# Kernel optimization log

Measured on AMD Instinct MI355X. Metric: run time of the kernel, lower is better.

## Reference

```python
import jax, jax.numpy as jnp
import numpy as np

# init_kwargs baked in as module constants
N, K, CONV_DIM = 20, 10, 512
T, ALPHA = 0.1, 0.1
BNORM = 1.0  # self.B == 2 only when N==K==5
BATCH = 256


def setup_inputs() -> dict:
    key = jax.random.key(0)
    op = jax.random.normal(key, (BATCH, N, K, 1, CONV_DIM), dtype=jnp.float32)
    return {"op": op}


def reference(op):
    # op: [B, N, K, 1, D]
    p = jnp.squeeze(op, axis=-2)                                  # [B,N,K,D]
    p = p / jnp.linalg.norm(p, axis=-1, keepdims=True)            # L2 normalize
    b = p.shape[0]
    all_p = p.reshape(b, N * K, CONV_DIM)                         # [B,NK,D] (n-major, k-minor, same as split+concat)

    # vectorized over all N*K anchors: pairwise similarities to all prototypes
    sims = jnp.einsum('bnkd,bmd->bnkm', p, all_p) / T             # [B,N,K,NK]
    self_sim = jnp.sum(p * p, axis=-1) / T                        # [B,N,K] (== 1/T after normalization)

    # denominator: sum of exp over all prototypes minus the anchor itself
    exp_term = jnp.sum(jnp.exp(sims), axis=-1) - jnp.exp(self_sim)  # [B,N,K]
    log_term = jnp.log(exp_term)

    # positive term: mean similarity to same-class prototypes excluding anchor
    pos = jnp.einsum('bnkd,bnjd->bnk', p, p) / T                  # sum over class members incl. self
    sum_term = (pos - self_sim) / (K - 1)                         # [B,N,K]

    cl_loss = jnp.sum(log_term - sum_term)                        # sums over batch and all anchors
    return ALPHA * cl_loss / (BNORM * N * K * CONV_DIM)
```

## Files before the change

kernel.cpp:

```cpp
#include <hip/hip_runtime.h>
#include <hip/hip_bf16.h>
#include <math.h>

#define BATCH   256
#define KMEM    10
#define NPROT   200
#define DDIM    512
#define TINVF   10.0f
#define KSLAB   64
#define NSLAB   (DDIM / KSLAB)
#define RPAD    256
#define ROWB    128
#define NSEG    800

typedef __attribute__((ext_vector_type(8))) short short8;
typedef __attribute__((ext_vector_type(4))) float f32x4;

__device__ __forceinline__ unsigned short f2bf(float v) {
    unsigned u = __float_as_uint(v);
    return (unsigned short)((u + 0x7fffu + ((u >> 16) & 1u)) >> 16);
}

__device__ __forceinline__ void pack16(const float4 c[4], uint4& p0, uint4& p1, float& sq) {
    union { unsigned short us[16]; uint4 u[2]; } w;
    const float* f = (const float*)c;
    #pragma unroll
    for (int e = 0; e < 16; e++) {
        float v = f[e];
        sq = fmaf(v, v, sq);
        w.us[e] = f2bf(v);
    }
    p0 = w.u[0];
    p1 = w.u[1];
}

__global__ __launch_bounds__(512, 2) void kmain(const float* __restrict__ P,
                                                float* __restrict__ partial) {
    __shared__ char  slab[2][RPAD * ROWB];
    __shared__ float normpart[NSEG];
    __shared__ float invn_s[RPAD];
    __shared__ float s1buf[2][RPAD];
    __shared__ float s2buf[2][RPAD];
    __shared__ float red[512];

    const int tid  = threadIdx.x;
    const int lane = tid & 63;
    const int wave = tid >> 6;
    const int wr   = wave >> 1;
    const int wc   = wave & 1;
    const int b    = blockIdx.x;
    const float* Pb = P + (size_t)b * NPROT * DDIM;

    for (int z = tid; z < 2 * 56 * 8; z += 512) {
        int bsel = z / (56 * 8);
        int slot = z % (56 * 8);
        int row  = NPROT + (slot >> 3);
        *(uint4*)(&slab[bsel][row * ROWB + (slot & 7) * 16]) = make_uint4(0, 0, 0, 0);
    }

    const int  idx0 = tid;
    const int  row0 = idx0 >> 2, seg0 = idx0 & 3;
    const int  idx1 = tid + 512;
    const bool has1 = (idx1 < NSEG);
    const int  row1 = idx1 >> 2, seg1 = idx1 & 3;

    float sq0 = 0.f, sq1 = 0.f;

    float4 curA[4], curB[4];
    {
        const float4* sA = (const float4*)(Pb + (size_t)row0 * DDIM + seg0 * 16);
        curA[0] = sA[0]; curA[1] = sA[1]; curA[2] = sA[2]; curA[3] = sA[3];
        if (has1) {
            const float4* sB = (const float4*)(Pb + (size_t)row1 * DDIM + seg1 * 16);
            curB[0] = sB[0]; curB[1] = sB[1]; curB[2] = sB[2]; curB[3] = sB[3];
        }
    }

    f32x4 acc[4][8];
    #pragma unroll
    for (int i = 0; i < 4; i++)
        #pragma unroll
        for (int j = 0; j < 8; j++)
            acc[i][j] = (f32x4)(0.f);

    const int swz0 = (row0 & 7) << 4;
    const int swz1 = (row1 & 7) << 4;

    for (int s = 0; s < NSLAB; s++) {
        char* buf = slab[s & 1];

        {
            uint4 p0, p1;
            pack16(curA, p0, p1, sq0);
            int byte0 = row0 * ROWB + seg0 * 32;
            *(uint4*)(&buf[(byte0     ) ^ swz0]) = p0;
            *(uint4*)(&buf[(byte0 + 16) ^ swz0]) = p1;
        }
        if (has1) {
            uint4 p0, p1;
            pack16(curB, p0, p1, sq1);
            int byte0 = row1 * ROWB + seg1 * 32;
            *(uint4*)(&buf[(byte0     ) ^ swz1]) = p0;
            *(uint4*)(&buf[(byte0 + 16) ^ swz1]) = p1;
        }
        __syncthreads();

        float4 nxtA[4], nxtB[4];
        if (s + 1 < NSLAB) {
            const float4* sA = (const float4*)(Pb + (size_t)row0 * DDIM + (s + 1) * KSLAB + seg0 * 16);
            nxtA[0] = sA[0]; nxtA[1] = sA[1]; nxtA[2] = sA[2]; nxtA[3] = sA[3];
            if (has1) {
                const float4* sB = (const float4*)(Pb + (size_t)row1 * DDIM + (s + 1) * KSLAB + seg1 * 16);
                nxtB[0] = sB[0]; nxtB[1] = sB[1]; nxtB[2] = sB[2]; nxtB[3] = sB[3];
            }
        }

        #pragma unroll
        for (int ks = 0; ks < 2; ks++) {
            const int kb = (ks * 32 + (lane >> 4) * 8) * 2;
            short8 af[4];
            #pragma unroll
            for (int i = 0; i < 4; i++) {
                int row = (wr * 4 + i) * 16 + (lane & 15);
                af[i] = *(const short8*)(&buf[(row * ROWB + kb) ^ ((row & 7) << 4)]);
            }
            #pragma unroll
            for (int j = 0; j < 8; j++) {
                int row = (wc * 8 + j) * 16 + (lane & 15);
                short8 bf = *(const short8*)(&buf[(row * ROWB + kb) ^ ((row & 7) << 4)]);
                #pragma unroll
                for (int i = 0; i < 4; i++)
                    acc[i][j] = __builtin_amdgcn_mfma_f32_16x16x32_bf16(af[i], bf, acc[i][j], 0, 0, 0);
            }
        }

        #pragma unroll
        for (int q = 0; q < 4; q++) { curA[q] = nxtA[q]; curB[q] = nxtB[q]; }
    }

    normpart[idx0] = sq0;
    if (has1) normpart[idx1] = sq1;
    __syncthreads();
    if (tid < RPAD) {
        float iv = 0.f;
        if (tid < NPROT) {
            float ns = normpart[4 * tid] + normpart[4 * tid + 1]
                     + normpart[4 * tid + 2] + normpart[4 * tid + 3];
            iv = rsqrtf(ns);
        }
        invn_s[tid] = iv;
    }
    __syncthreads();

    float ijn[8]; int jg[8], jdiv[8];
    #pragma unroll
    for (int j = 0; j < 8; j++) {
        jg[j]   = wc * 128 + j * 16 + (lane & 15);
        ijn[j]  = invn_s[jg[j]];
        jdiv[j] = jg[j] / KMEM;
    }
    #pragma unroll
    for (int i = 0; i < 4; i++) {
        #pragma unroll
        for (int r = 0; r < 4; r++) {
            const int m = wr * 64 + i * 16 + (lane >> 4) * 4 + r;
            const float im = invn_s[m];
            const int mdiv = m / KMEM;
            float s1 = 0.f, s2 = 0.f;
            #pragma unroll
            for (int j = 0; j < 8; j++) {
                float g = acc[i][j][r] * im * ijn[j];
                bool valid = (jg[j] < NPROT) && (m < NPROT) && (jg[j] != m);
                s1 += valid ? __expf(g * TINVF) : 0.f;
                s2 += (valid && (jdiv[j] == mdiv)) ? g : 0.f;
            }
            #pragma unroll
            for (int d = 1; d < 16; d <<= 1) {
                s1 += __shfl_xor(s1, d);
                s2 += __shfl_xor(s2, d);
            }
            if ((lane & 15) == 0) {
                s1buf[wc][m] = s1;
                s2buf[wc][m] = s2;
            }
        }
    }
    __syncthreads();

    float v = 0.f;
    if (tid < NPROT) {
        float S1 = s1buf[0][tid] + s1buf[1][tid];
        float S2 = s2buf[0][tid] + s2buf[1][tid];
        v = logf(S1) - S2 * (TINVF / 9.0f);
    }
    red[tid] = v;
    __syncthreads();
    for (int sx = 256; sx > 0; sx >>= 1) {
        if (tid < sx) red[tid] += red[tid + sx];
        __syncthreads();
    }
    if (tid == 0) partial[b] = red[0];
}

__global__ __launch_bounds__(256) void kfinal(const float* __restrict__ partial,
                                              float* __restrict__ out) {
    __shared__ double red[256];
    int tid = threadIdx.x;
    red[tid] = (double)partial[tid];
    __syncthreads();
    for (int sx = 128; sx > 0; sx >>= 1) {
        if (tid < sx) red[tid] += red[tid + sx];
        __syncthreads();
    }
    if (tid == 0) out[0] = (float)(red[0] * (0.1 / 102400.0));
}

extern "C" void kernel_launch(void* const* d_in, const int* in_sizes, int n_in,
                              void* d_out, int out_size, void* d_ws, size_t ws_size,
                              hipStream_t stream) {
    const float* P = (const float*)d_in[0];
    float* partial = (float*)d_ws;
    float* out     = (float*)d_out;

    kmain<<<BATCH, 512, 0, stream>>>(P, partial);
    kfinal<<<1, 256, 0, stream>>>(partial, out);
}
```

Baseline: 33.72 us.

## Split each batch element's similarity matrix across two blocks by row halves

Launches two blocks per batch element, each computing the MFMA tiles and loss terms for half of the anchor rows against all prototypes, and combines the doubled partial sums in the final reduction. This halves per-block compute and accumulator registers, and raises the occupancy hint, to increase parallelism across CUs. The cost is that both blocks load and convert the full input slab, duplicating global reads and bf16 packing work.

```diff
diff --git a/kernel.cpp b/kernel.cpp
--- a/kernel.cpp
+++ b/kernel.cpp
@@ -12,6 +12,7 @@
 #define RPAD    256
 #define ROWB    128
 #define NSEG    800
+#define NBLK    (BATCH * 2)
 
 typedef __attribute__((ext_vector_type(8))) short short8;
 typedef __attribute__((ext_vector_type(4))) float f32x4;
@@ -34,21 +35,22 @@
     p1 = w.u[1];
 }
 
-__global__ __launch_bounds__(512, 2) void kmain(const float* __restrict__ P,
+__global__ __launch_bounds__(512, 4) void kmain(const float* __restrict__ P,
                                                 float* __restrict__ partial) {
     __shared__ char  slab[2][RPAD * ROWB];
     __shared__ float normpart[NSEG];
     __shared__ float invn_s[RPAD];
-    __shared__ float s1buf[2][RPAD];
-    __shared__ float s2buf[2][RPAD];
+    __shared__ float s1buf[4][128];
+    __shared__ float s2buf[4][128];
     __shared__ float red[512];
 
     const int tid  = threadIdx.x;
     const int lane = tid & 63;
     const int wave = tid >> 6;
-    const int wr   = wave >> 1;
-    const int wc   = wave & 1;
-    const int b    = blockIdx.x;
+    const int wrh  = wave >> 2;
+    const int wcq  = wave & 3;
+    const int b    = blockIdx.x >> 1;
+    const int h    = blockIdx.x & 1;
     const float* Pb = P + (size_t)b * NPROT * DDIM;
 
     for (int z = tid; z < 2 * 56 * 8; z += 512) {
@@ -76,11 +78,11 @@
         }
     }
 
-    f32x4 acc[4][8];
+    f32x4 acc[4][4];
     #pragma unroll
     for (int i = 0; i < 4; i++)
         #pragma unroll
-        for (int j = 0; j < 8; j++)
+        for (int j = 0; j < 4; j++)
             acc[i][j] = (f32x4)(0.f);
 
     const int swz0 = (row0 & 7) << 4;
@@ -118,20 +120,22 @@
         #pragma unroll
         for (int ks = 0; ks < 2; ks++) {
             const int kb = (ks * 32 + (lane >> 4) * 8) * 2;
-            short8 af[4];
+            short8 af[4], bfr[4];
             #pragma unroll
             for (int i = 0; i < 4; i++) {
-                int row = (wr * 4 + i) * 16 + (lane & 15);
+                int row = (h * 8 + wrh * 4 + i) * 16 + (lane & 15);
                 af[i] = *(const short8*)(&buf[(row * ROWB + kb) ^ ((row & 7) << 4)]);
             }
             #pragma unroll
-            for (int j = 0; j < 8; j++) {
-                int row = (wc * 8 + j) * 16 + (lane & 15);
-                short8 bf = *(const short8*)(&buf[(row * ROWB + kb) ^ ((row & 7) << 4)]);
+            for (int j = 0; j < 4; j++) {
+                int row = (wcq * 4 + j) * 16 + (lane & 15);
+                bfr[j] = *(const short8*)(&buf[(row * ROWB + kb) ^ ((row & 7) << 4)]);
+            }
+            #pragma unroll
+            for (int j = 0; j < 4; j++)
                 #pragma unroll
                 for (int i = 0; i < 4; i++)
-                    acc[i][j] = __builtin_amdgcn_mfma_f32_16x16x32_bf16(af[i], bf, acc[i][j], 0, 0, 0);
-            }
+                    acc[i][j] = __builtin_amdgcn_mfma_f32_16x16x32_bf16(af[i], bfr[j], acc[i][j], 0, 0, 0);
         }
 
         #pragma unroll
@@ -152,10 +156,10 @@
     }
     __syncthreads();
 
-    float ijn[8]; int jg[8], jdiv[8];
-    #pragma unroll
-    for (int j = 0; j < 8; j++) {
-        jg[j]   = wc * 128 + j * 16 + (lane & 15);
+    float ijn[4]; int jg[4], jdiv[4];
+    #pragma unroll
+    for (int j = 0; j < 4; j++) {
+        jg[j]   = wcq * 64 + j * 16 + (lane & 15);
         ijn[j]  = invn_s[jg[j]];
         jdiv[j] = jg[j] / KMEM;
     }
@@ -163,12 +167,12 @@
     for (int i = 0; i < 4; i++) {
         #pragma unroll
         for (int r = 0; r < 4; r++) {
-            const int m = wr * 64 + i * 16 + (lane >> 4) * 4 + r;
+            const int m = h * 128 + wrh * 64 + i * 16 + (lane >> 4) * 4 + r;
             const float im = invn_s[m];
             const int mdiv = m / KMEM;
             float s1 = 0.f, s2 = 0.f;
             #pragma unroll
-            for (int j = 0; j < 8; j++) {
+            for (int j = 0; j < 4; j++) {
                 float g = acc[i][j][r] * im * ijn[j];
                 bool valid = (jg[j] < NPROT) && (m < NPROT) && (jg[j] != m);
                 s1 += valid ? __expf(g * TINVF) : 0.f;
@@ -180,18 +184,21 @@
                 s2 += __shfl_xor(s2, d);
             }
             if ((lane & 15) == 0) {
-                s1buf[wc][m] = s1;
-                s2buf[wc][m] = s2;
+                s1buf[wcq][m - h * 128] = s1;
+                s2buf[wcq][m - h * 128] = s2;
             }
         }
     }
     __syncthreads();
 
     float v = 0.f;
-    if (tid < NPROT) {
-        float S1 = s1buf[0][tid] + s1buf[1][tid];
-        float S2 = s2buf[0][tid] + s2buf[1][tid];
-        v = logf(S1) - S2 * (TINVF / 9.0f);
+    if (tid < 128) {
+        const int m = h * 128 + tid;
+        if (m < NPROT) {
+            float S1 = s1buf[0][tid] + s1buf[1][tid] + s1buf[2][tid] + s1buf[3][tid];
+            float S2 = s2buf[0][tid] + s2buf[1][tid] + s2buf[2][tid] + s2buf[3][tid];
+            v = logf(S1) - S2 * (TINVF / 9.0f);
+        }
     }
     red[tid] = v;
     __syncthreads();
@@ -199,14 +206,14 @@
         if (tid < sx) red[tid] += red[tid + sx];
         __syncthreads();
     }
-    if (tid == 0) partial[b] = red[0];
+    if (tid == 0) partial[blockIdx.x] = red[0];
 }
 
 __global__ __launch_bounds__(256) void kfinal(const float* __restrict__ partial,
                                               float* __restrict__ out) {
     __shared__ double red[256];
     int tid = threadIdx.x;
-    red[tid] = (double)partial[tid];
+    red[tid] = (double)partial[tid] + (double)partial[tid + 256];
     __syncthreads();
     for (int sx = 128; sx > 0; sx >>= 1) {
         if (tid < sx) red[tid] += red[tid + sx];
@@ -222,6 +229,6 @@
     float* partial = (float*)d_ws;
     float* out     = (float*)d_out;
 
-    kmain<<<BATCH, 512, 0, stream>>>(P, partial);
+    kmain<<<NBLK, 512, 0, stream>>>(P, partial);
     kfinal<<<1, 256, 0, stream>>>(partial, out);
 }
```

Result: slower. 94.77 us (+181.0%).

## Use 1024-thread blocks with 4x4 wave grid for Gram matrix tiles

Applied to the files above, without the earlier changes.

Doubles the block to 1024 threads (16 waves in a 4x4 grid), so each wave holds a 64x64 accumulator tile instead of 64x128. Each thread now converts one 16-float segment per slab instead of up to two. The aim is more wave-level parallelism and latency hiding per batch element, with fewer registers per thread. In exchange each wave reloads more A fragments relative to its MFMA work, the final reduction gets deeper, and the number of resident blocks per CU may drop.

```diff
diff --git a/kernel.cpp b/kernel.cpp
--- a/kernel.cpp
+++ b/kernel.cpp
@@ -34,85 +34,65 @@
     p1 = w.u[1];
 }
 
-__global__ __launch_bounds__(512, 2) void kmain(const float* __restrict__ P,
-                                                float* __restrict__ partial) {
+__global__ __launch_bounds__(1024) void kmain(const float* __restrict__ P,
+                                              float* __restrict__ partial) {
     __shared__ char  slab[2][RPAD * ROWB];
     __shared__ float normpart[NSEG];
     __shared__ float invn_s[RPAD];
-    __shared__ float s1buf[2][RPAD];
-    __shared__ float s2buf[2][RPAD];
-    __shared__ float red[512];
+    __shared__ float s1buf[4][RPAD];
+    __shared__ float s2buf[4][RPAD];
+    __shared__ float red[1024];
 
     const int tid  = threadIdx.x;
     const int lane = tid & 63;
     const int wave = tid >> 6;
-    const int wr   = wave >> 1;
-    const int wc   = wave & 1;
+    const int wr   = wave >> 2;
+    const int wc   = wave & 3;
     const int b    = blockIdx.x;
     const float* Pb = P + (size_t)b * NPROT * DDIM;
 
-    for (int z = tid; z < 2 * 56 * 8; z += 512) {
-        int bsel = z / (56 * 8);
-        int slot = z % (56 * 8);
+    if (tid < 2 * 56 * 8) {
+        int bsel = tid / (56 * 8);
+        int slot = tid % (56 * 8);
         int row  = NPROT + (slot >> 3);
         *(uint4*)(&slab[bsel][row * ROWB + (slot & 7) * 16]) = make_uint4(0, 0, 0, 0);
     }
 
-    const int  idx0 = tid;
-    const int  row0 = idx0 >> 2, seg0 = idx0 & 3;
-    const int  idx1 = tid + 512;
-    const bool has1 = (idx1 < NSEG);
-    const int  row1 = idx1 >> 2, seg1 = idx1 & 3;
-
-    float sq0 = 0.f, sq1 = 0.f;
-
-    float4 curA[4], curB[4];
-    {
+    const bool has0 = (tid < NSEG);
+    const int  row0 = tid >> 2, seg0 = tid & 3;
+    const int  swz0 = (row0 & 7) << 4;
+
+    float sq0 = 0.f;
+
+    float4 curA[4];
+    if (has0) {
         const float4* sA = (const float4*)(Pb + (size_t)row0 * DDIM + seg0 * 16);
         curA[0] = sA[0]; curA[1] = sA[1]; curA[2] = sA[2]; curA[3] = sA[3];
-        if (has1) {
-            const float4* sB = (const float4*)(Pb + (size_t)row1 * DDIM + seg1 * 16);
-            curB[0] = sB[0]; curB[1] = sB[1]; curB[2] = sB[2]; curB[3] = sB[3];
-        }
-    }
-
-    f32x4 acc[4][8];
+    }
+
+    f32x4 acc[4][4];
     #pragma unroll
     for (int i = 0; i < 4; i++)
         #pragma unroll
-        for (int j = 0; j < 8; j++)
+        for (int j = 0; j < 4; j++)
             acc[i][j] = (f32x4)(0.f);
-
-    const int swz0 = (row0 & 7) << 4;
-    const int swz1 = (row1 & 7) << 4;
 
     for (int s = 0; s < NSLAB; s++) {
         char* buf = slab[s & 1];
 
-        {
+        if (has0) {
             uint4 p0, p1;
             pack16(curA, p0, p1, sq0);
             int byte0 = row0 * ROWB + seg0 * 32;
             *(uint4*)(&buf[(byte0     ) ^ swz0]) = p0;
             *(uint4*)(&buf[(byte0 + 16) ^ swz0]) = p1;
         }
-        if (has1) {
-            uint4 p0, p1;
-            pack16(curB, p0, p1, sq1);
-            int byte0 = row1 * ROWB + seg1 * 32;
-            *(uint4*)(&buf[(byte0     ) ^ swz1]) = p0;
-            *(uint4*)(&buf[(byte0 + 16) ^ swz1]) = p1;
-        }
         __syncthreads();
 
-        float4 nxtA[4], nxtB[4];
-        if (s + 1 < NSLAB) {
+        float4 nxtA[4];
+        if (has0 && s + 1 < NSLAB) {
             const float4* sA = (const float4*)(Pb + (size_t)row0 * DDIM + (s + 1) * KSLAB + seg0 * 16);
             nxtA[0] = sA[0]; nxtA[1] = sA[1]; nxtA[2] = sA[2]; nxtA[3] = sA[3];
-            if (has1) {
-                const float4* sB = (const float4*)(Pb + (size_t)row1 * DDIM + (s + 1) * KSLAB + seg1 * 16);
-                nxtB[0] = sB[0]; nxtB[1] = sB[1]; nxtB[2] = sB[2]; nxtB[3] = sB[3];
-            }
         }
 
         #pragma unroll
@@ -125,21 +105,20 @@
                 af[i] = *(const short8*)(&buf[(row * ROWB + kb) ^ ((row & 7) << 4)]);
             }
             #pragma unroll
-            for (int j = 0; j < 8; j++) {
-                int row = (wc * 8 + j) * 16 + (lane & 15);
-                short8 bf = *(const short8*)(&buf[(row * ROWB + kb) ^ ((row & 7) << 4)]);
+            for (int j = 0; j < 4; j++) {
+                int row = (wc * 4 + j) * 16 + (lane & 15);
+                short8 bfr = *(const short8*)(&buf[(row * ROWB + kb) ^ ((row & 7) << 4)]);
                 #pragma unroll
                 for (int i = 0; i < 4; i++)
-                    acc[i][j] = __builtin_amdgcn_mfma_f32_16x16x32_bf16(af[i], bf, acc[i][j], 0, 0, 0);
-            }
-        }
-
-        #pragma unroll
-        for (int q = 0; q < 4; q++) { curA[q] = nxtA[q]; curB[q] = nxtB[q]; }
-    }
-
-    normpart[idx0] = sq0;
-    if (has1) normpart[idx1] = sq1;
+                    acc[i][j] = __builtin_amdgcn_mfma_f32_16x16x32_bf16(af[i], bfr, acc[i][j], 0, 0, 0);
+            }
+        }
+
+        #pragma unroll
+        for (int q = 0; q < 4; q++) curA[q] = nxtA[q];
+    }
+
+    if (has0) normpart[tid] = sq0;
     __syncthreads();
     if (tid < RPAD) {
         float iv = 0.f;
@@ -152,10 +131,10 @@
     }
     __syncthreads();
 
-    float ijn[8]; int jg[8], jdiv[8];
-    #pragma unroll
-    for (int j = 0; j < 8; j++) {
-        jg[j]   = wc * 128 + j * 16 + (lane & 15);
+    float ijn[4]; int jg[4], jdiv[4];
+    #pragma unroll
+    for (int j = 0; j < 4; j++) {
+        jg[j]   = wc * 64 + j * 16 + (lane & 15);
         ijn[j]  = invn_s[jg[j]];
         jdiv[j] = jg[j] / KMEM;
     }
@@ -168,7 +147,7 @@
             const int mdiv = m / KMEM;
             float s1 = 0.f, s2 = 0.f;
             #pragma unroll
-            for (int j = 0; j < 8; j++) {
+            for (int j = 0; j < 4; j++) {
                 float g = acc[i][j][r] * im * ijn[j];
                 bool valid = (jg[j] < NPROT) && (m < NPROT) && (jg[j] != m);
                 s1 += valid ? __expf(g * TINVF) : 0.f;
@@ -189,13 +168,13 @@
 
     float v = 0.f;
     if (tid < NPROT) {
-        float S1 = s1buf[0][tid] + s1buf[1][tid];
-        float S2 = s2buf[0][tid] + s2buf[1][tid];
+        float S1 = s1buf[0][tid] + s1buf[1][tid] + s1buf[2][tid] + s1buf[3][tid];
+        float S2 = s2buf[0][tid] + s2buf[1][tid] + s2buf[2][tid] + s2buf[3][tid];
         v = logf(S1) - S2 * (TINVF / 9.0f);
     }
     red[tid] = v;
     __syncthreads();
-    for (int sx = 256; sx > 0; sx >>= 1) {
+    for (int sx = 512; sx > 0; sx >>= 1) {
         if (tid < sx) red[tid] += red[tid + sx];
         __syncthreads();
     }
@@ -222,6 +201,6 @@
     float* partial = (float*)d_ws;
     float* out     = (float*)d_out;
 
-    kmain<<<BATCH, 512, 0, stream>>>(P, partial);
+    kmain<<<BATCH, 1024, 0, stream>>>(P, partial);
     kfinal<<<1, 256, 0, stream>>>(partial, out);
 }
```

Result: slower. 40.18 us (+19.2%).

## Deepen global prefetch to two slabs and use hardware bf16 pack conversion

Applied to the files above, without the earlier changes.

Each thread now holds two K-slabs of fp32 input in registers, so global loads run two slabs ahead of the MFMA compute instead of one. The loop is fully unrolled with fixed double-buffer phases, and the load for slab s+2 is issued before the barrier. The software round-to-nearest bf16 conversion is replaced by the v_cvt_pk_bf16_f32 instruction. The launch bound no longer asks for two blocks per CU, which gives the compiler more register room for the extra prefetch buffers but could lower occupancy.

```diff
diff --git a/kernel.cpp b/kernel.cpp
--- a/kernel.cpp
+++ b/kernel.cpp
@@ -16,26 +16,22 @@
 typedef __attribute__((ext_vector_type(8))) short short8;
 typedef __attribute__((ext_vector_type(4))) float f32x4;
 
-__device__ __forceinline__ unsigned short f2bf(float v) {
-    unsigned u = __float_as_uint(v);
-    return (unsigned short)((u + 0x7fffu + ((u >> 16) & 1u)) >> 16);
-}
-
-__device__ __forceinline__ void pack16(const float4 c[4], uint4& p0, uint4& p1, float& sq) {
-    union { unsigned short us[16]; uint4 u[2]; } w;
+__device__ __forceinline__ void pack16cvt(const float4 c[4], uint4& p0, uint4& p1, float& sq) {
     const float* f = (const float*)c;
-    #pragma unroll
-    for (int e = 0; e < 16; e++) {
-        float v = f[e];
-        sq = fmaf(v, v, sq);
-        w.us[e] = f2bf(v);
-    }
-    p0 = w.u[0];
-    p1 = w.u[1];
-}
-
-__global__ __launch_bounds__(512, 2) void kmain(const float* __restrict__ P,
-                                                float* __restrict__ partial) {
+    unsigned r[8];
+    #pragma unroll
+    for (int e = 0; e < 8; e++) {
+        float lo = f[2 * e], hi = f[2 * e + 1];
+        sq = fmaf(lo, lo, sq);
+        sq = fmaf(hi, hi, sq);
+        asm("v_cvt_pk_bf16_f32 %0, %1, %2" : "=v"(r[e]) : "v"(lo), "v"(hi));
+    }
+    p0 = make_uint4(r[0], r[1], r[2], r[3]);
+    p1 = make_uint4(r[4], r[5], r[6], r[7]);
+}
+
+__global__ __launch_bounds__(512) void kmain(const float* __restrict__ P,
+                                             float* __restrict__ partial) {
     __shared__ char  slab[2][RPAD * ROWB];
     __shared__ float normpart[NSEG];
     __shared__ float invn_s[RPAD];
@@ -63,16 +59,22 @@
     const int  idx1 = tid + 512;
     const bool has1 = (idx1 < NSEG);
     const int  row1 = idx1 >> 2, seg1 = idx1 & 3;
+    const int  swz0 = (row0 & 7) << 4;
+    const int  swz1 = (row1 & 7) << 4;
 
     float sq0 = 0.f, sq1 = 0.f;
 
-    float4 curA[4], curB[4];
+    float4 A0[4], A1[4], B0[4], B1[4];
     {
-        const float4* sA = (const float4*)(Pb + (size_t)row0 * DDIM + seg0 * 16);
-        curA[0] = sA[0]; curA[1] = sA[1]; curA[2] = sA[2]; curA[3] = sA[3];
+        const float4* s0 = (const float4*)(Pb + (size_t)row0 * DDIM + seg0 * 16);
+        A0[0] = s0[0]; A0[1] = s0[1]; A0[2] = s0[2]; A0[3] = s0[3];
+        const float4* s1p = (const float4*)(Pb + (size_t)row0 * DDIM + KSLAB + seg0 * 16);
+        B0[0] = s1p[0]; B0[1] = s1p[1]; B0[2] = s1p[2]; B0[3] = s1p[3];
         if (has1) {
-            const float4* sB = (const float4*)(Pb + (size_t)row1 * DDIM + seg1 * 16);
-            curB[0] = sB[0]; curB[1] = sB[1]; curB[2] = sB[2]; curB[3] = sB[3];
+            const float4* t0 = (const float4*)(Pb + (size_t)row1 * DDIM + seg1 * 16);
+            A1[0] = t0[0]; A1[1] = t0[1]; A1[2] = t0[2]; A1[3] = t0[3];
+            const float4* t1 = (const float4*)(Pb + (size_t)row1 * DDIM + KSLAB + seg1 * 16);
+            B1[0] = t1[0]; B1[1] = t1[1]; B1[2] = t1[2]; B1[3] = t1[3];
         }
     }
 
@@ -83,59 +85,59 @@
         for (int j = 0; j < 8; j++)
             acc[i][j] = (f32x4)(0.f);
 
-    const int swz0 = (row0 & 7) << 4;
-    const int swz1 = (row1 & 7) << 4;
-
-    for (int s = 0; s < NSLAB; s++) {
-        char* buf = slab[s & 1];
-
-        {
-            uint4 p0, p1;
-            pack16(curA, p0, p1, sq0);
-            int byte0 = row0 * ROWB + seg0 * 32;
-            *(uint4*)(&buf[(byte0     ) ^ swz0]) = p0;
-            *(uint4*)(&buf[(byte0 + 16) ^ swz0]) = p1;
-        }
-        if (has1) {
-            uint4 p0, p1;
-            pack16(curB, p0, p1, sq1);
-            int byte0 = row1 * ROWB + seg1 * 32;
-            *(uint4*)(&buf[(byte0     ) ^ swz1]) = p0;
-            *(uint4*)(&buf[(byte0 + 16) ^ swz1]) = p1;
-        }
-        __syncthreads();
-
-        float4 nxtA[4], nxtB[4];
-        if (s + 1 < NSLAB) {
-            const float4* sA = (const float4*)(Pb + (size_t)row0 * DDIM + (s + 1) * KSLAB + seg0 * 16);
-            nxtA[0] = sA[0]; nxtA[1] = sA[1]; nxtA[2] = sA[2]; nxtA[3] = sA[3];
+    #pragma unroll
+    for (int s2 = 0; s2 < NSLAB / 2; s2++) {
+        #pragma unroll
+        for (int ph = 0; ph < 2; ph++) {
+            const int s = 2 * s2 + ph;
+            char* buf = slab[ph];
+            float4* C0 = ph ? B0 : A0;
+            float4* C1 = ph ? B1 : A1;
+
+            {
+                uint4 p0, p1;
+                pack16cvt(C0, p0, p1, sq0);
+                int byte0 = row0 * ROWB + seg0 * 32;
+                *(uint4*)(&buf[(byte0     ) ^ swz0]) = p0;
+                *(uint4*)(&buf[(byte0 + 16) ^ swz0]) = p1;
+            }
             if (has1) {
-                const float4* sB = (const float4*)(Pb + (size_t)row1 * DDIM + (s + 1) * KSLAB + seg1 * 16);
-                nxtB[0] = sB[0]; nxtB[1] = sB[1]; nxtB[2] = sB[2]; nxtB[3] = sB[3];
-            }
-        }
-
-        #pragma unroll
-        for (int ks = 0; ks < 2; ks++) {
-            const int kb = (ks * 32 + (lane >> 4) * 8) * 2;
-            short8 af[4];
+                uint4 p0, p1;
+                pack16cvt(C1, p0, p1, sq1);
+                int byte0 = row1 * ROWB + seg1 * 32;
+                *(uint4*)(&buf[(byte0     ) ^ swz1]) = p0;
+                *(uint4*)(&buf[(byte0 + 16) ^ swz1]) = p1;
+            }
+
+            if (s + 2 < NSLAB) {
+                const float4* sA = (const float4*)(Pb + (size_t)row0 * DDIM + (s + 2) * KSLAB + seg0 * 16);
+                C0[0] = sA[0]; C0[1] = sA[1]; C0[2] = sA[2]; C0[3] = sA[3];
+                if (has1) {
+                    const float4* sB = (const float4*)(Pb + (size_t)row1 * DDIM + (s + 2) * KSLAB + seg1 * 16);
+                    C1[0] = sB[0]; C1[1] = sB[1]; C1[2] = sB[2]; C1[3] = sB[3];
+                }
+            }
+            __syncthreads();
+
             #pragma unroll
-            for (int i = 0; i < 4; i++) {
-                int row = (wr * 4 + i) * 16 + (lane & 15);
-                af[i] = *(const short8*)(&buf[(row * ROWB + kb) ^ ((row & 7) << 4)]);
-            }
-            #pragma unroll
-            for (int j = 0; j < 8; j++) {
-                int row = (wc * 8 + j) * 16 + (lane & 15);
-                short8 bf = *(const short8*)(&buf[(row * ROWB + kb) ^ ((row & 7) << 4)]);
+            for (int ks = 0; ks < 2; ks++) {
+                const int kb = (ks * 32 + (lane >> 4) * 8) * 2;
+                short8 af[4];
                 #pragma unroll
-                for (int i = 0; i < 4; i++)
-                    acc[i][j] = __builtin_amdgcn_mfma_f32_16x16x32_bf16(af[i], bf, acc[i][j], 0, 0, 0);
-            }
-        }
-
-        #pragma unroll
-        for (int q = 0; q < 4; q++) { curA[q] = nxtA[q]; curB[q] = nxtB[q]; }
+                for (int i = 0; i < 4; i++) {
+                    int row = (wr * 4 + i) * 16 + (lane & 15);
+                    af[i] = *(const short8*)(&buf[(row * ROWB + kb) ^ ((row & 7) << 4)]);
+                }
+                #pragma unroll
+                for (int j = 0; j < 8; j++) {
+                    int row = (wc * 8 + j) * 16 + (lane & 15);
+                    short8 bfr = *(const short8*)(&buf[(row * ROWB + kb) ^ ((row & 7) << 4)]);
+                    #pragma unroll
+                    for (int i = 0; i < 4; i++)
+                        acc[i][j] = __builtin_amdgcn_mfma_f32_16x16x32_bf16(af[i], bfr, acc[i][j], 0, 0, 0);
+                }
+            }
+        }
     }
 
     normpart[idx0] = sq0;
```

New measurement: 41.84 us. 1.24x slower.
